# Optimization experiments

Hardware: AMD Instinct MI355X
Metric: run time of the kernel (lower is better)

Reference implementation:

```python
import jax, jax.numpy as jnp
import numpy as np
from jax import lax

T, N, F, H, E = 8, 20000, 128, 256, 320000
LEAK = 0.9


def setup_inputs() -> dict:
    key = jax.random.key(0)
    k = jax.random.split(key, 7)
    x = jax.random.normal(k[0], (T, N, F), dtype=jnp.float32)
    edge_index = jax.random.randint(k[1], (2, E), 0, N, dtype=jnp.int32)
    # reservoir weights, scaled ~1/sqrt(fan_in) so tanh stays in its active range
    w_in0 = jax.random.normal(k[2], (H, F), dtype=jnp.float32) / jnp.sqrt(F)
    w_rec0 = jax.random.normal(k[3], (H, H), dtype=jnp.float32) / jnp.sqrt(H)
    w_in1 = jax.random.normal(k[4], (H, H), dtype=jnp.float32) / jnp.sqrt(H)
    w_rec1 = jax.random.normal(k[5], (H, H), dtype=jnp.float32) / jnp.sqrt(H)
    leakage = jnp.array(LEAK, dtype=jnp.float32)
    return {"x": x, "edge_index": edge_index, "w_in0": w_in0, "w_rec0": w_rec0,
            "w_in1": w_in1, "w_rec1": w_rec1, "leakage": leakage}


def reference(x, edge_index, w_in0, w_rec0, w_in1, w_rec1, leakage):
    # DynamicGraphReservoir with 2 ReservoirConvLayers, fixed graph over time,
    # zero initial states, no pooling, fully=False, return_sequences=False.
    src, dst = edge_index[0], edge_index[1]
    num_nodes = x.shape[1]

    def layer(w_in, w_rec, inp, state):
        # neighbour aggregation: sum_{(j->i) in E} state[j]   (scatter-add)
        agg = jax.ops.segment_sum(state[src], dst, num_segments=num_nodes)
        return leakage * jnp.tanh(inp @ w_in.T + agg @ w_rec.T) + (1.0 - leakage) * state

    def step(states, xt):
        s0, s1 = states
        s0 = layer(w_in0, w_rec0, xt, s0)   # layer 0 consumes input signal
        s1 = layer(w_in1, w_rec1, s0, s1)   # layer 1 consumes layer-0 state
        return (s0, s1), None

    init = (jnp.zeros((num_nodes, w_rec0.shape[0]), x.dtype),
            jnp.zeros((num_nodes, w_rec1.shape[0]), x.dtype))
    (s0, s1), _ = lax.scan(step, init, x)
    return s1  # final-layer final state: (nodes, hidden)
```

## Files before the change

kernel.cpp:

```cpp
#include <hip/hip_runtime.h>
#include <math.h>

#define T_STEPS 8
#define N_NODES 20000
#define F_IN    128
#define H_DIM   256
#define E_EDGES 320000

#define G_UPD    625
#define G_AGG    5000

typedef __attribute__((ext_vector_type(8))) short short8;
typedef __attribute__((ext_vector_type(4))) float f32x4;

__device__ __forceinline__ void split2(float v, unsigned short& h, unsigned short& l) {
    unsigned vi = __float_as_uint(v);
    h = (unsigned short)(vi >> 16);
    float hf = __uint_as_float(vi & 0xffff0000u);
    l = (unsigned short)(__float_as_uint(v - hf) >> 16);
}


__global__ void count_kernel(const int* __restrict__ dst, int* __restrict__ counts, int E) {
    int e = blockIdx.x * blockDim.x + threadIdx.x;
    if (e < E) atomicAdd(&counts[dst[e]], 1);
}

__global__ void scan_kernel(const int* __restrict__ counts, int* __restrict__ row_ptr,
                            int* __restrict__ cursors, int n) {
    __shared__ int buf[1024];
    __shared__ int carry_s;
    int tid = threadIdx.x;
    if (tid == 0) carry_s = 0;
    __syncthreads();
    for (int base = 0; base < n; base += 1024) {
        int i = base + tid;
        int v = (i < n) ? counts[i] : 0;
        buf[tid] = v;
        __syncthreads();
        for (int off = 1; off < 1024; off <<= 1) {
            int t = (tid >= off) ? buf[tid - off] : 0;
            __syncthreads();
            buf[tid] += t;
            __syncthreads();
        }
        int incl = buf[tid];
        int carry = carry_s;
        if (i < n) {
            int ex = carry + incl - v;
            row_ptr[i] = ex;
            cursors[i] = ex;
        }
        __syncthreads();
        if (tid == 1023) carry_s = carry + incl;
        __syncthreads();
    }
    if (tid == 0) row_ptr[n] = carry_s;
}

__global__ void fill_kernel(const int* __restrict__ src, const int* __restrict__ dst,
                            int* __restrict__ cursors, unsigned short* __restrict__ col, int E) {
    int e = blockIdx.x * blockDim.x + threadIdx.x;
    if (e < E) {
        int d = dst[e];
        int p = atomicAdd(&cursors[d], 1);
        col[p] = (unsigned short)src[e];
    }
}


__global__ void cvt_frag(const float* __restrict__ W, int K,
                         unsigned short* __restrict__ fh, unsigned short* __restrict__ fl) {
    int g = blockIdx.x * 256 + threadIdx.x;
    int KP32 = K >> 5;
    int total = (H_DIM / 16) * KP32 * 64;
    if (g >= total) return;
    int lane = g & 63;
    int kp = (g >> 6) % KP32;
    int rt = g / (KP32 << 6);
    int r = rt * 16 + (lane & 15);
    int c = kp * 32 + (lane >> 4) * 8;
    const float* p = W + (size_t)r * K + c;
    short8 h, l;
    #pragma unroll
    for (int j = 0; j < 8; ++j) {
        unsigned short hh, ll;
        split2(p[j], hh, ll);
        h[j] = (short)hh; l[j] = (short)ll;
    }
    *(short8*)(fh + (size_t)g * 8) = h;
    *(short8*)(fl + (size_t)g * 8) = l;
}


__global__ __launch_bounds__(256) void agg_kernel(
        const float* __restrict__ gsrcA, float* __restrict__ goutA,
        const float* __restrict__ gsrcB, float* __restrict__ goutB,
        const int* __restrict__ row_ptr, const unsigned short* __restrict__ col) {
    int b = blockIdx.x;
    const float* gsrc = gsrcA;
    float* gout = goutA;
    if (b >= G_AGG) { b -= G_AGG; gsrc = gsrcB; gout = goutB; }
    const int tid = threadIdx.x;
    const int lane = tid & 63, w = tid >> 6;
    const int chunk = b & 7;
    const int nb = b >> 3;
    const int slot = lane >> 3, comp = lane & 7;
    const float4* src4 = (const float4*)gsrc + (size_t)chunk * 8 + comp;
    const int r0 = nb * 32 + w * 8;

    int jj[8], en[8];
    float4 ac[8];
    #pragma unroll
    for (int k = 0; k < 8; ++k) {
        jj[k] = row_ptr[r0 + k] + slot;
        en[k] = row_ptr[r0 + k + 1];
        ac[k] = (float4){0.f, 0.f, 0.f, 0.f};
    }
    while (true) {
        bool ok[8];
        int ix[8];
        bool anyv = false;
        #pragma unroll
        for (int k = 0; k < 8; ++k) {
            ok[k] = jj[k] < en[k];
            anyv |= ok[k];
            ix[k] = ok[k] ? jj[k] : 0;
        }
        if (!anyv) break;
        int cc[8];
        #pragma unroll
        for (int k = 0; k < 8; ++k) cc[k] = col[ix[k]];
        #pragma unroll
        for (int k = 0; k < 8; ++k) {
            float4 v = src4[(size_t)cc[k] * 64];
            if (ok[k]) {
                ac[k].x += v.x; ac[k].y += v.y; ac[k].z += v.z; ac[k].w += v.w;
                jj[k] += 8;
            }
        }
    }
    #pragma unroll
    for (int k = 0; k < 8; ++k) {
        #pragma unroll
        for (int m = 8; m < 64; m <<= 1) {
            ac[k].x += __shfl_xor(ac[k].x, m);
            ac[k].y += __shfl_xor(ac[k].y, m);
            ac[k].z += __shfl_xor(ac[k].z, m);
            ac[k].w += __shfl_xor(ac[k].w, m);
        }
    }
    if (slot == 0) {
        #pragma unroll
        for (int k = 0; k < 8; ++k)
            *(float4*)(gout + (size_t)(r0 + k) * 256 + chunk * 32 + comp * 4) = ac[k];
    }
}


__device__ __forceinline__ void upd_body(
        const float* __restrict__ A1, int K1,
        const float* __restrict__ s_prev,
        const unsigned short* __restrict__ B1h, const unsigned short* __restrict__ B1l,
        const unsigned short* __restrict__ B2h, const unsigned short* __restrict__ B2l,
        const float* __restrict__ AGGu,
        float* __restrict__ s_new,
        const float* __restrict__ leak_ptr, int m0) {
    const int tid = threadIdx.x;
    const int lane = tid & 63, w = tid >> 6;
    const int fr = lane & 15, fq = lane >> 4;
    const int wn = w * 64;
    const int rtbase = w * 4;

    f32x4 acc[2][4];
    #pragma unroll
    for (int mi = 0; mi < 2; ++mi)
        #pragma unroll
        for (int nt = 0; nt < 4; ++nt)
            acc[mi][nt] = (f32x4){0.f, 0.f, 0.f, 0.f};

    {
        const int KP32 = K1 >> 5;
        const float* ar0 = A1 + (size_t)(m0 + fr) * K1 + fq * 8;
        const float* ar1 = A1 + (size_t)(m0 + 16 + fr) * K1 + fq * 8;
        float4 pA0, pA1, pB0, pB1;
        pA0 = *(const float4*)ar0;
        pA1 = *(const float4*)(ar0 + 4);
        pB0 = *(const float4*)ar1;
        pB1 = *(const float4*)(ar1 + 4);
        #pragma unroll 1
        for (int kp = 0; kp < KP32; ++kp) {
            const int kpn = (kp + 1 < KP32) ? kp + 1 : kp;
            float4 nA0 = *(const float4*)(ar0 + kpn * 32);
            float4 nA1 = *(const float4*)(ar0 + kpn * 32 + 4);
            float4 nB0 = *(const float4*)(ar1 + kpn * 32);
            float4 nB1 = *(const float4*)(ar1 + kpn * 32 + 4);
            short8 bh[4], bl[4];
            #pragma unroll
            for (int nt = 0; nt < 4; ++nt) {
                size_t off = ((size_t)((rtbase + nt) * KP32 + kp) * 64 + lane) * 8;
                bh[nt] = *(const short8*)(B1h + off);
                bl[nt] = *(const short8*)(B1l + off);
            }
            short8 ah[2], al[2];
            {
                unsigned short h, l;
                split2(pA0.x, h, l); ah[0][0] = (short)h; al[0][0] = (short)l;
                split2(pA0.y, h, l); ah[0][1] = (short)h; al[0][1] = (short)l;
                split2(pA0.z, h, l); ah[0][2] = (short)h; al[0][2] = (short)l;
                split2(pA0.w, h, l); ah[0][3] = (short)h; al[0][3] = (short)l;
                split2(pA1.x, h, l); ah[0][4] = (short)h; al[0][4] = (short)l;
                split2(pA1.y, h, l); ah[0][5] = (short)h; al[0][5] = (short)l;
                split2(pA1.z, h, l); ah[0][6] = (short)h; al[0][6] = (short)l;
                split2(pA1.w, h, l); ah[0][7] = (short)h; al[0][7] = (short)l;
                split2(pB0.x, h, l); ah[1][0] = (short)h; al[1][0] = (short)l;
                split2(pB0.y, h, l); ah[1][1] = (short)h; al[1][1] = (short)l;
                split2(pB0.z, h, l); ah[1][2] = (short)h; al[1][2] = (short)l;
                split2(pB0.w, h, l); ah[1][3] = (short)h; al[1][3] = (short)l;
                split2(pB1.x, h, l); ah[1][4] = (short)h; al[1][4] = (short)l;
                split2(pB1.y, h, l); ah[1][5] = (short)h; al[1][5] = (short)l;
                split2(pB1.z, h, l); ah[1][6] = (short)h; al[1][6] = (short)l;
                split2(pB1.w, h, l); ah[1][7] = (short)h; al[1][7] = (short)l;
            }
            #pragma unroll
            for (int mi = 0; mi < 2; ++mi)
                #pragma unroll
                for (int nt = 0; nt < 4; ++nt) {
                    f32x4 c = acc[mi][nt];
                    c = __builtin_amdgcn_mfma_f32_16x16x32_bf16(ah[mi], bh[nt], c, 0, 0, 0);
                    c = __builtin_amdgcn_mfma_f32_16x16x32_bf16(al[mi], bh[nt], c, 0, 0, 0);
                    c = __builtin_amdgcn_mfma_f32_16x16x32_bf16(ah[mi], bl[nt], c, 0, 0, 0);
                    acc[mi][nt] = c;
                }
            pA0 = nA0; pA1 = nA1; pB0 = nB0; pB1 = nB1;
        }
    }

    if (B2h) {
        const float* ar0 = AGGu + (size_t)(m0 + fr) * H_DIM + fq * 8;
        const float* ar1 = AGGu + (size_t)(m0 + 16 + fr) * H_DIM + fq * 8;
        float4 pA0, pA1, pB0, pB1;
        pA0 = *(const float4*)ar0;
        pA1 = *(const float4*)(ar0 + 4);
        pB0 = *(const float4*)ar1;
        pB1 = *(const float4*)(ar1 + 4);
        #pragma unroll 1
        for (int kp = 0; kp < 8; ++kp) {
            const int kpn = (kp + 1 < 8) ? kp + 1 : kp;
            float4 nA0 = *(const float4*)(ar0 + kpn * 32);
            float4 nA1 = *(const float4*)(ar0 + kpn * 32 + 4);
            float4 nB0 = *(const float4*)(ar1 + kpn * 32);
            float4 nB1 = *(const float4*)(ar1 + kpn * 32 + 4);
            short8 bh[4], bl[4];
            #pragma unroll
            for (int nt = 0; nt < 4; ++nt) {
                size_t off = ((size_t)((rtbase + nt) * 8 + kp) * 64 + lane) * 8;
                bh[nt] = *(const short8*)(B2h + off);
                bl[nt] = *(const short8*)(B2l + off);
            }
            short8 ah[2], al[2];
            {
                unsigned short h, l;
                split2(pA0.x, h, l); ah[0][0] = (short)h; al[0][0] = (short)l;
                split2(pA0.y, h, l); ah[0][1] = (short)h; al[0][1] = (short)l;
                split2(pA0.z, h, l); ah[0][2] = (short)h; al[0][2] = (short)l;
                split2(pA0.w, h, l); ah[0][3] = (short)h; al[0][3] = (short)l;
                split2(pA1.x, h, l); ah[0][4] = (short)h; al[0][4] = (short)l;
                split2(pA1.y, h, l); ah[0][5] = (short)h; al[0][5] = (short)l;
                split2(pA1.z, h, l); ah[0][6] = (short)h; al[0][6] = (short)l;
                split2(pA1.w, h, l); ah[0][7] = (short)h; al[0][7] = (short)l;
                split2(pB0.x, h, l); ah[1][0] = (short)h; al[1][0] = (short)l;
                split2(pB0.y, h, l); ah[1][1] = (short)h; al[1][1] = (short)l;
                split2(pB0.z, h, l); ah[1][2] = (short)h; al[1][2] = (short)l;
                split2(pB0.w, h, l); ah[1][3] = (short)h; al[1][3] = (short)l;
                split2(pB1.x, h, l); ah[1][4] = (short)h; al[1][4] = (short)l;
                split2(pB1.y, h, l); ah[1][5] = (short)h; al[1][5] = (short)l;
                split2(pB1.z, h, l); ah[1][6] = (short)h; al[1][6] = (short)l;
                split2(pB1.w, h, l); ah[1][7] = (short)h; al[1][7] = (short)l;
            }
            #pragma unroll
            for (int mi = 0; mi < 2; ++mi)
                #pragma unroll
                for (int nt = 0; nt < 4; ++nt) {
                    f32x4 c = acc[mi][nt];
                    c = __builtin_amdgcn_mfma_f32_16x16x32_bf16(ah[mi], bh[nt], c, 0, 0, 0);
                    c = __builtin_amdgcn_mfma_f32_16x16x32_bf16(al[mi], bh[nt], c, 0, 0, 0);
                    c = __builtin_amdgcn_mfma_f32_16x16x32_bf16(ah[mi], bl[nt], c, 0, 0, 0);
                    acc[mi][nt] = c;
                }
            pA0 = nA0; pA1 = nA1; pB0 = nB0; pB1 = nB1;
        }
    }

    const float leak = leak_ptr[0], il = 1.0f - leak;
    #pragma unroll
    for (int mi = 0; mi < 2; ++mi)
        #pragma unroll
        for (int r = 0; r < 4; ++r) {
            int m = m0 + mi * 16 + fq * 4 + r;
            #pragma unroll
            for (int nt = 0; nt < 4; ++nt) {
                int n = wn + nt * 16 + fr;
                size_t idx = (size_t)m * H_DIM + n;
                float old = s_prev[idx];
                float pre = acc[mi][nt][r];
                float e = __expf(2.0f * pre);
                float th = 1.0f - 2.0f / (e + 1.0f);
                s_new[idx] = leak * th + il * old;
            }
        }
}

__global__ __launch_bounds__(256) void upd_kernel(
        const float* __restrict__ A1a, int K1a, const float* __restrict__ spa,
        const unsigned short* __restrict__ B1ha, const unsigned short* __restrict__ B1la,
        const unsigned short* __restrict__ B2ha, const unsigned short* __restrict__ B2la,
        const float* __restrict__ AGGa, float* __restrict__ sna,
        const float* __restrict__ A1b, int K1b, const float* __restrict__ spb,
        const unsigned short* __restrict__ B1hb, const unsigned short* __restrict__ B1lb,
        const unsigned short* __restrict__ B2hb, const unsigned short* __restrict__ B2lb,
        const float* __restrict__ AGGb, float* __restrict__ snb,
        const float* __restrict__ leak_ptr, int merged) {
    if (merged) {
        const int task = blockIdx.x & 1;
        const int m0 = (blockIdx.x >> 1) * 32;
        if (task == 0)
            upd_body(A1a, K1a, spa, B1ha, B1la, B2ha, B2la, AGGa, sna, leak_ptr, m0);
        else
            upd_body(A1b, K1b, spb, B1hb, B1lb, B2hb, B2lb, AGGb, snb, leak_ptr, m0);
    } else {
        upd_body(A1a, K1a, spa, B1ha, B1la, B2ha, B2la, AGGa, sna, leak_ptr, blockIdx.x * 32);
    }
}


extern "C" void kernel_launch(void* const* d_in, const int* in_sizes, int n_in,
                              void* d_out, int out_size, void* d_ws, size_t ws_size,
                              hipStream_t stream) {
    const float* x        = (const float*)d_in[0];
    const int*   edge     = (const int*)d_in[1];
    const float* w_in0    = (const float*)d_in[2];
    const float* w_rec0   = (const float*)d_in[3];
    const float* w_in1    = (const float*)d_in[4];
    const float* w_rec1   = (const float*)d_in[5];
    const float* leak_ptr = (const float*)d_in[6];

    const int* src = edge;
    const int* dst = edge + E_EDGES;

    char* ws = (char*)d_ws;
    size_t off = 0;
    auto alloc = [&](size_t bytes) -> char* {
        char* p = ws + off;
        off += (bytes + 255) & ~(size_t)255;
        return p;
    };
    const size_t state_bytes = (size_t)N_NODES * H_DIM * sizeof(float);
    float* s0b[2]; float* s1b[2];
    s0b[0] = (float*)alloc(state_bytes);
    s0b[1] = (float*)alloc(state_bytes);
    s1b[0] = (float*)d_out;
    s1b[1] = (float*)alloc(state_bytes);
    float* AGG0 = (float*)alloc(state_bytes);
    float* AGG1 = (float*)alloc(state_bytes);
    unsigned short* w0h  = (unsigned short*)alloc(256 * 128 * 2);
    unsigned short* w0l  = (unsigned short*)alloc(256 * 128 * 2);
    unsigned short* wr0h = (unsigned short*)alloc(256 * 256 * 2);
    unsigned short* wr0l = (unsigned short*)alloc(256 * 256 * 2);
    unsigned short* w1h  = (unsigned short*)alloc(256 * 256 * 2);
    unsigned short* w1l  = (unsigned short*)alloc(256 * 256 * 2);
    unsigned short* wr1h = (unsigned short*)alloc(256 * 256 * 2);
    unsigned short* wr1l = (unsigned short*)alloc(256 * 256 * 2);
    int* row_ptr = (int*)alloc((N_NODES + 1) * sizeof(int));
    int* cursors = (int*)alloc(N_NODES * sizeof(int));
    int* counts  = (int*)alloc(N_NODES * sizeof(int));
    unsigned short* col = (unsigned short*)alloc((size_t)E_EDGES * sizeof(unsigned short));

    hipMemsetAsync(s0b[0], 0, state_bytes, stream);
    hipMemsetAsync(s1b[0], 0, state_bytes, stream);
    hipMemsetAsync(counts, 0, N_NODES * sizeof(int), stream);

    cvt_frag<<<16, 256, 0, stream>>>(w_in0, F_IN, w0h, w0l);
    cvt_frag<<<32, 256, 0, stream>>>(w_rec0, H_DIM, wr0h, wr0l);
    cvt_frag<<<32, 256, 0, stream>>>(w_in1, H_DIM, w1h, w1l);
    cvt_frag<<<32, 256, 0, stream>>>(w_rec1, H_DIM, wr1h, wr1l);

    count_kernel<<<(E_EDGES + 255) / 256, 256, 0, stream>>>(dst, counts, E_EDGES);
    scan_kernel<<<1, 1024, 0, stream>>>(counts, row_ptr, cursors, N_NODES);
    fill_kernel<<<(E_EDGES + 255) / 256, 256, 0, stream>>>(src, dst, cursors, col, E_EDGES);

    dim3 g_upd1(G_UPD);
    dim3 g_upd2(2 * G_UPD);
    dim3 g_agg1(G_AGG);
    dim3 g_agg2(2 * G_AGG);


    upd_kernel<<<g_upd1, 256, 0, stream>>>(
        x, F_IN, s0b[0], w0h, w0l, nullptr, nullptr, nullptr, s0b[1],
        nullptr, 0, nullptr, nullptr, nullptr, nullptr, nullptr, nullptr, nullptr,
        leak_ptr, 0);
    agg_kernel<<<g_agg1, 256, 0, stream>>>(s0b[1], AGG0, nullptr, nullptr, row_ptr, col);

    for (int t = 0; t < 7; ++t) {
        const float* s0_t  = s0b[(t + 1) & 1];
        float* s0_n        = s0b[t & 1];
        const float* s1_p  = s1b[t & 1];
        float* s1_t        = s1b[(t + 1) & 1];
        const float* xt1 = x + (size_t)(t + 1) * N_NODES * F_IN;
        int dg1 = (t > 0) ? 1 : 0;

        upd_kernel<<<g_upd2, 256, 0, stream>>>(
            s0_t, H_DIM, s1_p, w1h, w1l,
            dg1 ? wr1h : nullptr, dg1 ? wr1l : nullptr, AGG1, s1_t,
            xt1, F_IN, s0_t, w0h, w0l, wr0h, wr0l, AGG0, s0_n,
            leak_ptr, 1);

        if (t < 6) {
            agg_kernel<<<g_agg2, 256, 0, stream>>>(s1_t, AGG1, s0_n, AGG0, row_ptr, col);
        } else {
            agg_kernel<<<g_agg1, 256, 0, stream>>>(s1_t, AGG1, nullptr, nullptr, row_ptr, col);
        }
    }

    upd_kernel<<<g_upd1, 256, 0, stream>>>(
        s0b[0], H_DIM, s1b[1], w1h, w1l, wr1h, wr1l, AGG1, s1b[0],
        nullptr, 0, nullptr, nullptr, nullptr, nullptr, nullptr, nullptr, nullptr,
        leak_ptr, 0);
}
```

Baseline: 1.298 ms.

## Store state copies in column-chunked layout for cache-friendly neighbor gathers

The update kernel now also writes each new state into a chunk-major copy (8 chunks of 32 columns, each N×32 contiguous). The aggregation kernel gathers from that copy and writes AGG in the same chunked layout, which the update kernel reads back. Each aggregation block touches only one 2.5MB chunk, so random neighbor gathers should stay cache-resident instead of striding over the full 20MB state. The cost is an extra full-state write per update with scattered 4-byte stores, plus two extra state buffers.

```diff
diff --git a/kernel.cpp b/kernel.cpp
--- a/kernel.cpp
+++ b/kernel.cpp
@@ -9,6 +9,7 @@
 
 #define G_UPD    625
 #define G_AGG    5000
+#define N32      ((size_t)N_NODES * 32)
 
 typedef __attribute__((ext_vector_type(8))) short short8;
 typedef __attribute__((ext_vector_type(4))) float f32x4;
@@ -106,7 +107,7 @@
     const int chunk = b & 7;
     const int nb = b >> 3;
     const int slot = lane >> 3, comp = lane & 7;
-    const float4* src4 = (const float4*)gsrc + (size_t)chunk * 8 + comp;
+    const float4* src4 = (const float4*)gsrc + (size_t)chunk * (N32 / 4) + comp;
     const int r0 = nb * 32 + w * 8;
 
     int jj[8], en[8];
@@ -133,7 +134,7 @@
         for (int k = 0; k < 8; ++k) cc[k] = col[ix[k]];
         #pragma unroll
         for (int k = 0; k < 8; ++k) {
-            float4 v = src4[(size_t)cc[k] * 64];
+            float4 v = src4[(size_t)cc[k] * 8];
             if (ok[k]) {
                 ac[k].x += v.x; ac[k].y += v.y; ac[k].z += v.z; ac[k].w += v.w;
                 jj[k] += 8;
@@ -153,7 +154,7 @@
     if (slot == 0) {
         #pragma unroll
         for (int k = 0; k < 8; ++k)
-            *(float4*)(gout + (size_t)(r0 + k) * 256 + chunk * 32 + comp * 4) = ac[k];
+            *(float4*)(gout + (size_t)chunk * N32 + (size_t)(r0 + k) * 32 + comp * 4) = ac[k];
     }
 }
 
@@ -164,7 +165,7 @@
         const unsigned short* __restrict__ B1h, const unsigned short* __restrict__ B1l,
         const unsigned short* __restrict__ B2h, const unsigned short* __restrict__ B2l,
         const float* __restrict__ AGGu,
-        float* __restrict__ s_new,
+        float* __restrict__ s_new, float* __restrict__ s_new_cm,
         const float* __restrict__ leak_ptr, int m0) {
     const int tid = threadIdx.x;
     const int lane = tid & 63, w = tid >> 6;
@@ -237,20 +238,20 @@
     }
 
     if (B2h) {
-        const float* ar0 = AGGu + (size_t)(m0 + fr) * H_DIM + fq * 8;
-        const float* ar1 = AGGu + (size_t)(m0 + 16 + fr) * H_DIM + fq * 8;
+        const float* a0base = AGGu + (size_t)(m0 + fr) * 32 + fq * 8;
+        const float* a1base = AGGu + (size_t)(m0 + 16 + fr) * 32 + fq * 8;
         float4 pA0, pA1, pB0, pB1;
-        pA0 = *(const float4*)ar0;
-        pA1 = *(const float4*)(ar0 + 4);
-        pB0 = *(const float4*)ar1;
-        pB1 = *(const float4*)(ar1 + 4);
+        pA0 = *(const float4*)a0base;
+        pA1 = *(const float4*)(a0base + 4);
+        pB0 = *(const float4*)a1base;
+        pB1 = *(const float4*)(a1base + 4);
         #pragma unroll 1
         for (int kp = 0; kp < 8; ++kp) {
-            const int kpn = (kp + 1 < 8) ? kp + 1 : kp;
-            float4 nA0 = *(const float4*)(ar0 + kpn * 32);
-            float4 nA1 = *(const float4*)(ar0 + kpn * 32 + 4);
-            float4 nB0 = *(const float4*)(ar1 + kpn * 32);
-            float4 nB1 = *(const float4*)(ar1 + kpn * 32 + 4);
+            const size_t offn = (size_t)((kp + 1 < 8) ? kp + 1 : kp) * N32;
+            float4 nA0 = *(const float4*)(a0base + offn);
+            float4 nA1 = *(const float4*)(a0base + offn + 4);
+            float4 nB0 = *(const float4*)(a1base + offn);
+            float4 nB1 = *(const float4*)(a1base + offn + 4);
             short8 bh[4], bl[4];
             #pragma unroll
             for (int nt = 0; nt < 4; ++nt) {
@@ -306,7 +307,9 @@
                 float pre = acc[mi][nt][r];
                 float e = __expf(2.0f * pre);
                 float th = 1.0f - 2.0f / (e + 1.0f);
-                s_new[idx] = leak * th + il * old;
+                float val = leak * th + il * old;
+                s_new[idx] = val;
+                s_new_cm[(size_t)(n >> 5) * N32 + (size_t)m * 32 + (n & 31)] = val;
             }
         }
 }
@@ -315,21 +318,22 @@
         const float* __restrict__ A1a, int K1a, const float* __restrict__ spa,
         const unsigned short* __restrict__ B1ha, const unsigned short* __restrict__ B1la,
         const unsigned short* __restrict__ B2ha, const unsigned short* __restrict__ B2la,
-        const float* __restrict__ AGGa, float* __restrict__ sna,
+        const float* __restrict__ AGGa, float* __restrict__ sna, float* __restrict__ snacm,
         const float* __restrict__ A1b, int K1b, const float* __restrict__ spb,
         const unsigned short* __restrict__ B1hb, const unsigned short* __restrict__ B1lb,
         const unsigned short* __restrict__ B2hb, const unsigned short* __restrict__ B2lb,
-        const float* __restrict__ AGGb, float* __restrict__ snb,
+        const float* __restrict__ AGGb, float* __restrict__ snb, float* __restrict__ snbcm,
         const float* __restrict__ leak_ptr, int merged) {
     if (merged) {
         const int task = blockIdx.x & 1;
         const int m0 = (blockIdx.x >> 1) * 32;
         if (task == 0)
-            upd_body(A1a, K1a, spa, B1ha, B1la, B2ha, B2la, AGGa, sna, leak_ptr, m0);
+            upd_body(A1a, K1a, spa, B1ha, B1la, B2ha, B2la, AGGa, sna, snacm, leak_ptr, m0);
         else
-            upd_body(A1b, K1b, spb, B1hb, B1lb, B2hb, B2lb, AGGb, snb, leak_ptr, m0);
+            upd_body(A1b, K1b, spb, B1hb, B1lb, B2hb, B2lb, AGGb, snb, snbcm, leak_ptr, m0);
     } else {
-        upd_body(A1a, K1a, spa, B1ha, B1la, B2ha, B2la, AGGa, sna, leak_ptr, blockIdx.x * 32);
+        upd_body(A1a, K1a, spa, B1ha, B1la, B2ha, B2la, AGGa, sna, snacm, leak_ptr,
+                 blockIdx.x * 32);
     }
 }
 
@@ -361,6 +365,8 @@
     s0b[1] = (float*)alloc(state_bytes);
     s1b[0] = (float*)d_out;
     s1b[1] = (float*)alloc(state_bytes);
+    float* s0cm = (float*)alloc(state_bytes);
+    float* s1cm = (float*)alloc(state_bytes);
     float* AGG0 = (float*)alloc(state_bytes);
     float* AGG1 = (float*)alloc(state_bytes);
     unsigned short* w0h  = (unsigned short*)alloc(256 * 128 * 2);
@@ -396,10 +402,10 @@
 
 
     upd_kernel<<<g_upd1, 256, 0, stream>>>(
-        x, F_IN, s0b[0], w0h, w0l, nullptr, nullptr, nullptr, s0b[1],
-        nullptr, 0, nullptr, nullptr, nullptr, nullptr, nullptr, nullptr, nullptr,
+        x, F_IN, s0b[0], w0h, w0l, nullptr, nullptr, nullptr, s0b[1], s0cm,
+        nullptr, 0, nullptr, nullptr, nullptr, nullptr, nullptr, nullptr, nullptr, nullptr,
         leak_ptr, 0);
-    agg_kernel<<<g_agg1, 256, 0, stream>>>(s0b[1], AGG0, nullptr, nullptr, row_ptr, col);
+    agg_kernel<<<g_agg1, 256, 0, stream>>>(s0cm, AGG0, nullptr, nullptr, row_ptr, col);
 
     for (int t = 0; t < 7; ++t) {
         const float* s0_t  = s0b[(t + 1) & 1];
@@ -411,19 +417,19 @@
 
         upd_kernel<<<g_upd2, 256, 0, stream>>>(
             s0_t, H_DIM, s1_p, w1h, w1l,
-            dg1 ? wr1h : nullptr, dg1 ? wr1l : nullptr, AGG1, s1_t,
-            xt1, F_IN, s0_t, w0h, w0l, wr0h, wr0l, AGG0, s0_n,
+            dg1 ? wr1h : nullptr, dg1 ? wr1l : nullptr, AGG1, s1_t, s1cm,
+            xt1, F_IN, s0_t, w0h, w0l, wr0h, wr0l, AGG0, s0_n, s0cm,
             leak_ptr, 1);
 
         if (t < 6) {
-            agg_kernel<<<g_agg2, 256, 0, stream>>>(s1_t, AGG1, s0_n, AGG0, row_ptr, col);
+            agg_kernel<<<g_agg2, 256, 0, stream>>>(s1cm, AGG1, s0cm, AGG0, row_ptr, col);
         } else {
-            agg_kernel<<<g_agg1, 256, 0, stream>>>(s1_t, AGG1, nullptr, nullptr, row_ptr, col);
+            agg_kernel<<<g_agg1, 256, 0, stream>>>(s1cm, AGG1, nullptr, nullptr, row_ptr, col);
         }
     }
 
     upd_kernel<<<g_upd1, 256, 0, stream>>>(
-        s0b[0], H_DIM, s1b[1], w1h, w1l, wr1h, wr1l, AGG1, s1b[0],
-        nullptr, 0, nullptr, nullptr, nullptr, nullptr, nullptr, nullptr, nullptr,
+        s0b[0], H_DIM, s1b[1], w1h, w1l, wr1h, wr1l, AGG1, s1b[0], s1cm,
+        nullptr, 0, nullptr, nullptr, nullptr, nullptr, nullptr, nullptr, nullptr, nullptr,
         leak_ptr, 0);
 }
```

Result: slower. 1.336 ms (+2.9%).

## Store states as bf16 hi/lo pairs and gather int16 fixed-point chunked copies

Applied to the files above, without the earlier changes.

States, aggregates and the input sequence are now kept as pre-split bf16 hi/lo arrays, so the update kernel no longer splits fp32 operands inside its MFMA loop. The update epilogue also writes an int16 fixed-point copy of each state in a chunk-major layout, and the aggregation kernel gathers these 8-byte vectors and sums them in integers. This cuts gather bytes per edge by half and improves locality. The cost is quantization error in the neighbour sums (scale 1/32768, clamped), an extra pass that converts the whole input, and more output streams per update.

```diff
diff --git a/kernel.cpp b/kernel.cpp
--- a/kernel.cpp
+++ b/kernel.cpp
@@ -9,8 +9,11 @@
 
 #define G_UPD    625
 #define G_AGG    5000
+#define NC32     ((size_t)N_NODES * 32)
 
 typedef __attribute__((ext_vector_type(8))) short short8;
+typedef __attribute__((ext_vector_type(4))) short s16x4;
+typedef __attribute__((ext_vector_type(4))) unsigned short us4;
 typedef __attribute__((ext_vector_type(4))) float f32x4;
 
 __device__ __forceinline__ void split2(float v, unsigned short& h, unsigned short& l) {
@@ -18,6 +21,10 @@
     h = (unsigned short)(vi >> 16);
     float hf = __uint_as_float(vi & 0xffff0000u);
     l = (unsigned short)(__float_as_uint(v - hf) >> 16);
+}
+
+__device__ __forceinline__ float bf2f(unsigned short h) {
+    return __uint_as_float((unsigned)h << 16);
 }
 
 
@@ -93,29 +100,48 @@
 }
 
 
+__global__ void cvt_split(const float* __restrict__ src, unsigned short* __restrict__ dh,
+                          unsigned short* __restrict__ dl, int total4) {
+    int g = blockIdx.x * 256 + threadIdx.x;
+    if (g >= total4) return;
+    float4 v = *(const float4*)(src + (size_t)g * 4);
+    us4 h, l;
+    unsigned short hh, ll;
+    split2(v.x, hh, ll); h[0] = hh; l[0] = ll;
+    split2(v.y, hh, ll); h[1] = hh; l[1] = ll;
+    split2(v.z, hh, ll); h[2] = hh; l[2] = ll;
+    split2(v.w, hh, ll); h[3] = hh; l[3] = ll;
+    *(us4*)(dh + (size_t)g * 4) = h;
+    *(us4*)(dl + (size_t)g * 4) = l;
+}
+
+
 __global__ __launch_bounds__(256) void agg_kernel(
-        const float* __restrict__ gsrcA, float* __restrict__ goutA,
-        const float* __restrict__ gsrcB, float* __restrict__ goutB,
+        const short* __restrict__ gsrcA,
+        unsigned short* __restrict__ goAh, unsigned short* __restrict__ goAl,
+        const short* __restrict__ gsrcB,
+        unsigned short* __restrict__ goBh, unsigned short* __restrict__ goBl,
         const int* __restrict__ row_ptr, const unsigned short* __restrict__ col) {
     int b = blockIdx.x;
-    const float* gsrc = gsrcA;
-    float* gout = goutA;
-    if (b >= G_AGG) { b -= G_AGG; gsrc = gsrcB; gout = goutB; }
+    const short* gsrc = gsrcA;
+    unsigned short* goh = goAh;
+    unsigned short* gol = goAl;
+    if (b >= G_AGG) { b -= G_AGG; gsrc = gsrcB; goh = goBh; gol = goBl; }
     const int tid = threadIdx.x;
     const int lane = tid & 63, w = tid >> 6;
     const int chunk = b & 7;
     const int nb = b >> 3;
     const int slot = lane >> 3, comp = lane & 7;
-    const float4* src4 = (const float4*)gsrc + (size_t)chunk * 8 + comp;
+    const s16x4* src4 = (const s16x4*)(gsrc + (size_t)chunk * NC32) + comp;
     const int r0 = nb * 32 + w * 8;
 
     int jj[8], en[8];
-    float4 ac[8];
+    int ac[8][4];
     #pragma unroll
     for (int k = 0; k < 8; ++k) {
         jj[k] = row_ptr[r0 + k] + slot;
         en[k] = row_ptr[r0 + k + 1];
-        ac[k] = (float4){0.f, 0.f, 0.f, 0.f};
+        ac[k][0] = 0; ac[k][1] = 0; ac[k][2] = 0; ac[k][3] = 0;
     }
     while (true) {
         bool ok[8];
@@ -133,9 +159,12 @@
         for (int k = 0; k < 8; ++k) cc[k] = col[ix[k]];
         #pragma unroll
         for (int k = 0; k < 8; ++k) {
-            float4 v = src4[(size_t)cc[k] * 64];
+            s16x4 v = src4[(size_t)cc[k] * 8];
             if (ok[k]) {
-                ac[k].x += v.x; ac[k].y += v.y; ac[k].z += v.z; ac[k].w += v.w;
+                ac[k][0] += (int)v[0];
+                ac[k][1] += (int)v[1];
+                ac[k][2] += (int)v[2];
+                ac[k][3] += (int)v[3];
                 jj[k] += 8;
             }
         }
@@ -144,27 +173,38 @@
     for (int k = 0; k < 8; ++k) {
         #pragma unroll
         for (int m = 8; m < 64; m <<= 1) {
-            ac[k].x += __shfl_xor(ac[k].x, m);
-            ac[k].y += __shfl_xor(ac[k].y, m);
-            ac[k].z += __shfl_xor(ac[k].z, m);
-            ac[k].w += __shfl_xor(ac[k].w, m);
+            ac[k][0] += __shfl_xor(ac[k][0], m);
+            ac[k][1] += __shfl_xor(ac[k][1], m);
+            ac[k][2] += __shfl_xor(ac[k][2], m);
+            ac[k][3] += __shfl_xor(ac[k][3], m);
         }
     }
     if (slot == 0) {
-        #pragma unroll
-        for (int k = 0; k < 8; ++k)
-            *(float4*)(gout + (size_t)(r0 + k) * 256 + chunk * 32 + comp * 4) = ac[k];
+        const float sc = 1.0f / 32768.0f;
+        #pragma unroll
+        for (int k = 0; k < 8; ++k) {
+            us4 h, l;
+            unsigned short hh, ll;
+            split2((float)ac[k][0] * sc, hh, ll); h[0] = hh; l[0] = ll;
+            split2((float)ac[k][1] * sc, hh, ll); h[1] = hh; l[1] = ll;
+            split2((float)ac[k][2] * sc, hh, ll); h[2] = hh; l[2] = ll;
+            split2((float)ac[k][3] * sc, hh, ll); h[3] = hh; l[3] = ll;
+            size_t o = (size_t)(r0 + k) * H_DIM + chunk * 32 + comp * 4;
+            *(us4*)(goh + o) = h;
+            *(us4*)(gol + o) = l;
+        }
     }
 }
 
 
 __device__ __forceinline__ void upd_body(
-        const float* __restrict__ A1, int K1,
-        const float* __restrict__ s_prev,
+        const unsigned short* __restrict__ Ahi, const unsigned short* __restrict__ Alo, int K1,
+        const unsigned short* __restrict__ sphi, const unsigned short* __restrict__ splo,
         const unsigned short* __restrict__ B1h, const unsigned short* __restrict__ B1l,
         const unsigned short* __restrict__ B2h, const unsigned short* __restrict__ B2l,
-        const float* __restrict__ AGGu,
-        float* __restrict__ s_new,
+        const unsigned short* __restrict__ AGh, const unsigned short* __restrict__ AGl,
+        unsigned short* __restrict__ snhi, unsigned short* __restrict__ snlo,
+        short* __restrict__ sncm, float* __restrict__ dout,
         const float* __restrict__ leak_ptr, int m0) {
     const int tid = threadIdx.x;
     const int lane = tid & 63, w = tid >> 6;
@@ -181,46 +221,28 @@
 
     {
         const int KP32 = K1 >> 5;
-        const float* ar0 = A1 + (size_t)(m0 + fr) * K1 + fq * 8;
-        const float* ar1 = A1 + (size_t)(m0 + 16 + fr) * K1 + fq * 8;
-        float4 pA0, pA1, pB0, pB1;
-        pA0 = *(const float4*)ar0;
-        pA1 = *(const float4*)(ar0 + 4);
-        pB0 = *(const float4*)ar1;
-        pB1 = *(const float4*)(ar1 + 4);
+        const unsigned short* ah0p = Ahi + (size_t)(m0 + fr) * K1 + fq * 8;
+        const unsigned short* ah1p = Ahi + (size_t)(m0 + 16 + fr) * K1 + fq * 8;
+        const unsigned short* al0p = Alo + (size_t)(m0 + fr) * K1 + fq * 8;
+        const unsigned short* al1p = Alo + (size_t)(m0 + 16 + fr) * K1 + fq * 8;
+        short8 ah[2], al[2];
+        ah[0] = *(const short8*)ah0p;
+        ah[1] = *(const short8*)ah1p;
+        al[0] = *(const short8*)al0p;
+        al[1] = *(const short8*)al1p;
         #pragma unroll 1
         for (int kp = 0; kp < KP32; ++kp) {
             const int kpn = (kp + 1 < KP32) ? kp + 1 : kp;
-            float4 nA0 = *(const float4*)(ar0 + kpn * 32);
-            float4 nA1 = *(const float4*)(ar0 + kpn * 32 + 4);
-            float4 nB0 = *(const float4*)(ar1 + kpn * 32);
-            float4 nB1 = *(const float4*)(ar1 + kpn * 32 + 4);
+            short8 nh0 = *(const short8*)(ah0p + kpn * 32);
+            short8 nh1 = *(const short8*)(ah1p + kpn * 32);
+            short8 nl0 = *(const short8*)(al0p + kpn * 32);
+            short8 nl1 = *(const short8*)(al1p + kpn * 32);
             short8 bh[4], bl[4];
             #pragma unroll
             for (int nt = 0; nt < 4; ++nt) {
                 size_t off = ((size_t)((rtbase + nt) * KP32 + kp) * 64 + lane) * 8;
                 bh[nt] = *(const short8*)(B1h + off);
                 bl[nt] = *(const short8*)(B1l + off);
-            }
-            short8 ah[2], al[2];
-            {
-                unsigned short h, l;
-                split2(pA0.x, h, l); ah[0][0] = (short)h; al[0][0] = (short)l;
-                split2(pA0.y, h, l); ah[0][1] = (short)h; al[0][1] = (short)l;
-                split2(pA0.z, h, l); ah[0][2] = (short)h; al[0][2] = (short)l;
-                split2(pA0.w, h, l); ah[0][3] = (short)h; al[0][3] = (short)l;
-                split2(pA1.x, h, l); ah[0][4] = (short)h; al[0][4] = (short)l;
-                split2(pA1.y, h, l); ah[0][5] = (short)h; al[0][5] = (short)l;
-                split2(pA1.z, h, l); ah[0][6] = (short)h; al[0][6] = (short)l;
-                split2(pA1.w, h, l); ah[0][7] = (short)h; al[0][7] = (short)l;
-                split2(pB0.x, h, l); ah[1][0] = (short)h; al[1][0] = (short)l;
-                split2(pB0.y, h, l); ah[1][1] = (short)h; al[1][1] = (short)l;
-                split2(pB0.z, h, l); ah[1][2] = (short)h; al[1][2] = (short)l;
-                split2(pB0.w, h, l); ah[1][3] = (short)h; al[1][3] = (short)l;
-                split2(pB1.x, h, l); ah[1][4] = (short)h; al[1][4] = (short)l;
-                split2(pB1.y, h, l); ah[1][5] = (short)h; al[1][5] = (short)l;
-                split2(pB1.z, h, l); ah[1][6] = (short)h; al[1][6] = (short)l;
-                split2(pB1.w, h, l); ah[1][7] = (short)h; al[1][7] = (short)l;
             }
             #pragma unroll
             for (int mi = 0; mi < 2; ++mi)
@@ -232,51 +254,33 @@
                     c = __builtin_amdgcn_mfma_f32_16x16x32_bf16(ah[mi], bl[nt], c, 0, 0, 0);
                     acc[mi][nt] = c;
                 }
-            pA0 = nA0; pA1 = nA1; pB0 = nB0; pB1 = nB1;
+            ah[0] = nh0; ah[1] = nh1; al[0] = nl0; al[1] = nl1;
         }
     }
 
     if (B2h) {
-        const float* ar0 = AGGu + (size_t)(m0 + fr) * H_DIM + fq * 8;
-        const float* ar1 = AGGu + (size_t)(m0 + 16 + fr) * H_DIM + fq * 8;
-        float4 pA0, pA1, pB0, pB1;
-        pA0 = *(const float4*)ar0;
-        pA1 = *(const float4*)(ar0 + 4);
-        pB0 = *(const float4*)ar1;
-        pB1 = *(const float4*)(ar1 + 4);
+        const unsigned short* ah0p = AGh + (size_t)(m0 + fr) * H_DIM + fq * 8;
+        const unsigned short* ah1p = AGh + (size_t)(m0 + 16 + fr) * H_DIM + fq * 8;
+        const unsigned short* al0p = AGl + (size_t)(m0 + fr) * H_DIM + fq * 8;
+        const unsigned short* al1p = AGl + (size_t)(m0 + 16 + fr) * H_DIM + fq * 8;
+        short8 ah[2], al[2];
+        ah[0] = *(const short8*)ah0p;
+        ah[1] = *(const short8*)ah1p;
+        al[0] = *(const short8*)al0p;
+        al[1] = *(const short8*)al1p;
         #pragma unroll 1
         for (int kp = 0; kp < 8; ++kp) {
             const int kpn = (kp + 1 < 8) ? kp + 1 : kp;
-            float4 nA0 = *(const float4*)(ar0 + kpn * 32);
-            float4 nA1 = *(const float4*)(ar0 + kpn * 32 + 4);
-            float4 nB0 = *(const float4*)(ar1 + kpn * 32);
-            float4 nB1 = *(const float4*)(ar1 + kpn * 32 + 4);
+            short8 nh0 = *(const short8*)(ah0p + kpn * 32);
+            short8 nh1 = *(const short8*)(ah1p + kpn * 32);
+            short8 nl0 = *(const short8*)(al0p + kpn * 32);
+            short8 nl1 = *(const short8*)(al1p + kpn * 32);
             short8 bh[4], bl[4];
             #pragma unroll
             for (int nt = 0; nt < 4; ++nt) {
                 size_t off = ((size_t)((rtbase + nt) * 8 + kp) * 64 + lane) * 8;
                 bh[nt] = *(const short8*)(B2h + off);
                 bl[nt] = *(const short8*)(B2l + off);
-            }
-            short8 ah[2], al[2];
-            {
-                unsigned short h, l;
-                split2(pA0.x, h, l); ah[0][0] = (short)h; al[0][0] = (short)l;
-                split2(pA0.y, h, l); ah[0][1] = (short)h; al[0][1] = (short)l;
-                split2(pA0.z, h, l); ah[0][2] = (short)h; al[0][2] = (short)l;
-                split2(pA0.w, h, l); ah[0][3] = (short)h; al[0][3] = (short)l;
-                split2(pA1.x, h, l); ah[0][4] = (short)h; al[0][4] = (short)l;
-                split2(pA1.y, h, l); ah[0][5] = (short)h; al[0][5] = (short)l;
-                split2(pA1.z, h, l); ah[0][6] = (short)h; al[0][6] = (short)l;
-                split2(pA1.w, h, l); ah[0][7] = (short)h; al[0][7] = (short)l;
-                split2(pB0.x, h, l); ah[1][0] = (short)h; al[1][0] = (short)l;
-                split2(pB0.y, h, l); ah[1][1] = (short)h; al[1][1] = (short)l;
-                split2(pB0.z, h, l); ah[1][2] = (short)h; al[1][2] = (short)l;
-                split2(pB0.w, h, l); ah[1][3] = (short)h; al[1][3] = (short)l;
-                split2(pB1.x, h, l); ah[1][4] = (short)h; al[1][4] = (short)l;
-                split2(pB1.y, h, l); ah[1][5] = (short)h; al[1][5] = (short)l;
-                split2(pB1.z, h, l); ah[1][6] = (short)h; al[1][6] = (short)l;
-                split2(pB1.w, h, l); ah[1][7] = (short)h; al[1][7] = (short)l;
             }
             #pragma unroll
             for (int mi = 0; mi < 2; ++mi)
@@ -288,7 +292,7 @@
                     c = __builtin_amdgcn_mfma_f32_16x16x32_bf16(ah[mi], bl[nt], c, 0, 0, 0);
                     acc[mi][nt] = c;
                 }
-            pA0 = nA0; pA1 = nA1; pB0 = nB0; pB1 = nB1;
+            ah[0] = nh0; ah[1] = nh1; al[0] = nl0; al[1] = nl1;
         }
     }
 
@@ -302,34 +306,51 @@
             for (int nt = 0; nt < 4; ++nt) {
                 int n = wn + nt * 16 + fr;
                 size_t idx = (size_t)m * H_DIM + n;
-                float old = s_prev[idx];
+                float old = bf2f(sphi[idx]) + bf2f(splo[idx]);
                 float pre = acc[mi][nt][r];
                 float e = __expf(2.0f * pre);
                 float th = 1.0f - 2.0f / (e + 1.0f);
-                s_new[idx] = leak * th + il * old;
+                float val = leak * th + il * old;
+                unsigned short hh, ll;
+                split2(val, hh, ll);
+                snhi[idx] = hh;
+                snlo[idx] = ll;
+                int q = __float2int_rn(val * 32768.0f);
+                q = q > 32767 ? 32767 : (q < -32767 ? -32767 : q);
+                sncm[(size_t)(n >> 5) * NC32 + (size_t)m * 32 + (n & 31)] = (short)q;
+                if (dout) dout[idx] = val;
             }
         }
 }
 
 __global__ __launch_bounds__(256) void upd_kernel(
-        const float* __restrict__ A1a, int K1a, const float* __restrict__ spa,
+        const unsigned short* __restrict__ Aha, const unsigned short* __restrict__ Ala, int Ka,
+        const unsigned short* __restrict__ spha, const unsigned short* __restrict__ spla,
         const unsigned short* __restrict__ B1ha, const unsigned short* __restrict__ B1la,
         const unsigned short* __restrict__ B2ha, const unsigned short* __restrict__ B2la,
-        const float* __restrict__ AGGa, float* __restrict__ sna,
-        const float* __restrict__ A1b, int K1b, const float* __restrict__ spb,
+        const unsigned short* __restrict__ AGha, const unsigned short* __restrict__ AGla,
+        unsigned short* __restrict__ snha, unsigned short* __restrict__ snla,
+        short* __restrict__ scma, float* __restrict__ douta,
+        const unsigned short* __restrict__ Ahb, const unsigned short* __restrict__ Alb, int Kb,
+        const unsigned short* __restrict__ sphb, const unsigned short* __restrict__ splb,
         const unsigned short* __restrict__ B1hb, const unsigned short* __restrict__ B1lb,
         const unsigned short* __restrict__ B2hb, const unsigned short* __restrict__ B2lb,
-        const float* __restrict__ AGGb, float* __restrict__ snb,
+        const unsigned short* __restrict__ AGhb, const unsigned short* __restrict__ AGlb,
+        unsigned short* __restrict__ snhb, unsigned short* __restrict__ snlb,
+        short* __restrict__ scmb, float* __restrict__ doutb,
         const float* __restrict__ leak_ptr, int merged) {
     if (merged) {
         const int task = blockIdx.x & 1;
         const int m0 = (blockIdx.x >> 1) * 32;
         if (task == 0)
-            upd_body(A1a, K1a, spa, B1ha, B1la, B2ha, B2la, AGGa, sna, leak_ptr, m0);
+            upd_body(Aha, Ala, Ka, spha, spla, B1ha, B1la, B2ha, B2la,
+                     AGha, AGla, snha, snla, scma, douta, leak_ptr, m0);
         else
-            upd_body(A1b, K1b, spb, B1hb, B1lb, B2hb, B2lb, AGGb, snb, leak_ptr, m0);
+            upd_body(Ahb, Alb, Kb, sphb, splb, B1hb, B1lb, B2hb, B2lb,
+                     AGhb, AGlb, snhb, snlb, scmb, doutb, leak_ptr, m0);
     } else {
-        upd_body(A1a, K1a, spa, B1ha, B1la, B2ha, B2la, AGGa, sna, leak_ptr, blockIdx.x * 32);
+        upd_body(Aha, Ala, Ka, spha, spla, B1ha, B1la, B2ha, B2la,
+                 AGha, AGla, snha, snla, scma, douta, leak_ptr, blockIdx.x * 32);
     }
 }
 
@@ -355,14 +376,27 @@
         off += (bytes + 255) & ~(size_t)255;
         return p;
     };
-    const size_t state_bytes = (size_t)N_NODES * H_DIM * sizeof(float);
-    float* s0b[2]; float* s1b[2];
-    s0b[0] = (float*)alloc(state_bytes);
-    s0b[1] = (float*)alloc(state_bytes);
-    s1b[0] = (float*)d_out;
-    s1b[1] = (float*)alloc(state_bytes);
-    float* AGG0 = (float*)alloc(state_bytes);
-    float* AGG1 = (float*)alloc(state_bytes);
+    const size_t sh_bytes = (size_t)N_NODES * H_DIM * sizeof(unsigned short);
+    const size_t x_bytes  = (size_t)T_STEPS * N_NODES * F_IN * sizeof(unsigned short);
+
+    unsigned short* s0h[2]; unsigned short* s0l[2];
+    unsigned short* s1h[2]; unsigned short* s1l[2];
+    s0h[0] = (unsigned short*)alloc(sh_bytes);
+    s0h[1] = (unsigned short*)alloc(sh_bytes);
+    s0l[0] = (unsigned short*)alloc(sh_bytes);
+    s0l[1] = (unsigned short*)alloc(sh_bytes);
+    s1h[0] = (unsigned short*)alloc(sh_bytes);
+    s1h[1] = (unsigned short*)alloc(sh_bytes);
+    s1l[0] = (unsigned short*)alloc(sh_bytes);
+    s1l[1] = (unsigned short*)alloc(sh_bytes);
+    short* s0cm = (short*)alloc(sh_bytes);
+    short* s1cm = (short*)alloc(sh_bytes);
+    unsigned short* AG0h = (unsigned short*)alloc(sh_bytes);
+    unsigned short* AG0l = (unsigned short*)alloc(sh_bytes);
+    unsigned short* AG1h = (unsigned short*)alloc(sh_bytes);
+    unsigned short* AG1l = (unsigned short*)alloc(sh_bytes);
+    unsigned short* xh   = (unsigned short*)alloc(x_bytes);
+    unsigned short* xl   = (unsigned short*)alloc(x_bytes);
     unsigned short* w0h  = (unsigned short*)alloc(256 * 128 * 2);
     unsigned short* w0l  = (unsigned short*)alloc(256 * 128 * 2);
     unsigned short* wr0h = (unsigned short*)alloc(256 * 256 * 2);
@@ -376,14 +410,17 @@
     int* counts  = (int*)alloc(N_NODES * sizeof(int));
     unsigned short* col = (unsigned short*)alloc((size_t)E_EDGES * sizeof(unsigned short));
 
-    hipMemsetAsync(s0b[0], 0, state_bytes, stream);
-    hipMemsetAsync(s1b[0], 0, state_bytes, stream);
+    hipMemsetAsync(s0h[0], 0, sh_bytes, stream);
+    hipMemsetAsync(s0l[0], 0, sh_bytes, stream);
+    hipMemsetAsync(s1h[0], 0, sh_bytes, stream);
+    hipMemsetAsync(s1l[0], 0, sh_bytes, stream);
     hipMemsetAsync(counts, 0, N_NODES * sizeof(int), stream);
 
     cvt_frag<<<16, 256, 0, stream>>>(w_in0, F_IN, w0h, w0l);
     cvt_frag<<<32, 256, 0, stream>>>(w_rec0, H_DIM, wr0h, wr0l);
     cvt_frag<<<32, 256, 0, stream>>>(w_in1, H_DIM, w1h, w1l);
     cvt_frag<<<32, 256, 0, stream>>>(w_rec1, H_DIM, wr1h, wr1l);
+    cvt_split<<<20000, 256, 0, stream>>>(x, xh, xl, T_STEPS * N_NODES * F_IN / 4);
 
     count_kernel<<<(E_EDGES + 255) / 256, 256, 0, stream>>>(dst, counts, E_EDGES);
     scan_kernel<<<1, 1024, 0, stream>>>(counts, row_ptr, cursors, N_NODES);
@@ -394,36 +431,51 @@
     dim3 g_agg1(G_AGG);
     dim3 g_agg2(2 * G_AGG);
 
+    const size_t xstep = (size_t)N_NODES * F_IN;
+
 
     upd_kernel<<<g_upd1, 256, 0, stream>>>(
-        x, F_IN, s0b[0], w0h, w0l, nullptr, nullptr, nullptr, s0b[1],
-        nullptr, 0, nullptr, nullptr, nullptr, nullptr, nullptr, nullptr, nullptr,
+        xh, xl, F_IN, s0h[0], s0l[0], w0h, w0l, nullptr, nullptr,
+        nullptr, nullptr, s0h[1], s0l[1], s0cm, nullptr,
+        nullptr, nullptr, 0, nullptr, nullptr, nullptr, nullptr, nullptr, nullptr,
+        nullptr, nullptr, nullptr, nullptr, nullptr, nullptr,
         leak_ptr, 0);
-    agg_kernel<<<g_agg1, 256, 0, stream>>>(s0b[1], AGG0, nullptr, nullptr, row_ptr, col);
+    agg_kernel<<<g_agg1, 256, 0, stream>>>(s0cm, AG0h, AG0l,
+                                           nullptr, nullptr, nullptr, row_ptr, col);
 
     for (int t = 0; t < 7; ++t) {
-        const float* s0_t  = s0b[(t + 1) & 1];
-        float* s0_n        = s0b[t & 1];
-        const float* s1_p  = s1b[t & 1];
-        float* s1_t        = s1b[(t + 1) & 1];
-        const float* xt1 = x + (size_t)(t + 1) * N_NODES * F_IN;
+        unsigned short* s0th = s0h[(t + 1) & 1];
+        unsigned short* s0tl = s0l[(t + 1) & 1];
+        unsigned short* s0nh = s0h[t & 1];
+        unsigned short* s0nl = s0l[t & 1];
+        unsigned short* s1ph = s1h[t & 1];
+        unsigned short* s1pl = s1l[t & 1];
+        unsigned short* s1th = s1h[(t + 1) & 1];
+        unsigned short* s1tl = s1l[(t + 1) & 1];
         int dg1 = (t > 0) ? 1 : 0;
 
         upd_kernel<<<g_upd2, 256, 0, stream>>>(
-            s0_t, H_DIM, s1_p, w1h, w1l,
-            dg1 ? wr1h : nullptr, dg1 ? wr1l : nullptr, AGG1, s1_t,
-            xt1, F_IN, s0_t, w0h, w0l, wr0h, wr0l, AGG0, s0_n,
+            s0th, s0tl, H_DIM, s1ph, s1pl, w1h, w1l,
+            dg1 ? wr1h : nullptr, dg1 ? wr1l : nullptr,
+            AG1h, AG1l, s1th, s1tl, s1cm, nullptr,
+            xh + (size_t)(t + 1) * xstep, xl + (size_t)(t + 1) * xstep, F_IN,
+            s0th, s0tl, w0h, w0l, wr0h, wr0l,
+            AG0h, AG0l, s0nh, s0nl, s0cm, nullptr,
             leak_ptr, 1);
 
         if (t < 6) {
-            agg_kernel<<<g_agg2, 256, 0, stream>>>(s1_t, AGG1, s0_n, AGG0, row_ptr, col);
+            agg_kernel<<<g_agg2, 256, 0, stream>>>(s1cm, AG1h, AG1l,
+                                                   s0cm, AG0h, AG0l, row_ptr, col);
         } else {
-            agg_kernel<<<g_agg1, 256, 0, stream>>>(s1_t, AGG1, nullptr, nullptr, row_ptr, col);
+            agg_kernel<<<g_agg1, 256, 0, stream>>>(s1cm, AG1h, AG1l,
+                                                   nullptr, nullptr, nullptr, row_ptr, col);
         }
     }
 
     upd_kernel<<<g_upd1, 256, 0, stream>>>(
-        s0b[0], H_DIM, s1b[1], w1h, w1l, wr1h, wr1l, AGG1, s1b[0],
-        nullptr, 0, nullptr, nullptr, nullptr, nullptr, nullptr, nullptr, nullptr,
+        s0h[0], s0l[0], H_DIM, s1h[1], s1l[1], w1h, w1l, wr1h, wr1l,
+        AG1h, AG1l, s1h[0], s1l[0], s1cm, (float*)d_out,
+        nullptr, nullptr, 0, nullptr, nullptr, nullptr, nullptr, nullptr, nullptr,
+        nullptr, nullptr, nullptr, nullptr, nullptr, nullptr,
         leak_ptr, 0);
 }
```

Measured after the change: 1.437 ms. 1.11x slower.
